# Kernel optimization log

Measured on AMD Instinct MI355X. Metric: run time of the kernel, lower is better.

The kernel has to match this reference:

```python
import jax, jax.numpy as jnp
from jax import lax
import numpy as np

N_STEPS = 6  # fixed-grid dopri5 steps over t in [0,1] (stands in for adaptive solve at rtol=atol=1e-3)
EPS = 1e-5


def group_norm(x, w, b, groups=32):
    B, C, H, W = x.shape
    xr = x.reshape(B, groups, -1)
    m = xr.mean(-1, keepdims=True)
    v = xr.var(-1, keepdims=True)
    xn = ((xr - m) * lax.rsqrt(v + EPS)).reshape(B, C, H, W)
    return xn * w[None, :, None, None] + b[None, :, None, None]


def conv2d(x, w, b, stride, pad):
    y = lax.conv_general_dilated(x, w, (stride, stride), [(pad, pad), (pad, pad)],
                                 dimension_numbers=('NCHW', 'OIHW', 'NCHW'))
    return y + b[None, :, None, None]


def make_odefunc(oa_w, oa_b, occ1_w, occ1_b, ob_w, ob_b, occ2_w, occ2_b, oc_w, oc_b):
    def f(t, x):
        B, _, H, W = x.shape
        tt = jnp.full((B, 1, H, W), t, x.dtype)
        h = jax.nn.relu(group_norm(x, oa_w, oa_b))
        h = conv2d(jnp.concatenate([tt, h], axis=1), occ1_w, occ1_b, 1, 1)
        h = jax.nn.relu(group_norm(h, ob_w, ob_b))
        h = conv2d(jnp.concatenate([tt, h], axis=1), occ2_w, occ2_b, 1, 1)
        return group_norm(h, oc_w, oc_b)
    return f


def dopri5_fixed(f, y0, t0=0.0, t1=1.0, n=N_STEPS):
    h = (t1 - t0) / n
    def step(y, i):
        t = t0 + i * h
        k1 = f(t, y)
        k2 = f(t + h * (1/5),  y + h * (1/5) * k1)
        k3 = f(t + h * (3/10), y + h * ((3/40) * k1 + (9/40) * k2))
        k4 = f(t + h * (4/5),  y + h * ((44/45) * k1 + (-56/15) * k2 + (32/9) * k3))
        k5 = f(t + h * (8/9),  y + h * ((19372/6561) * k1 + (-25360/2187) * k2 + (64448/6561) * k3 + (-212/729) * k4))
        k6 = f(t + h,          y + h * ((9017/3168) * k1 + (-355/33) * k2 + (46732/5247) * k3 + (49/176) * k4 + (-5103/18656) * k5))
        y1 = y + h * ((35/384) * k1 + (500/1113) * k3 + (125/192) * k4 + (-2187/6784) * k5 + (11/84) * k6)
        return y1, None
    y, _ = lax.scan(step, y0, jnp.arange(n, dtype=jnp.float32))
    return y


def setup_inputs() -> dict:
    key = jax.random.key(0)
    ks = jax.random.split(key, 8)
    d = {}
    d['x'] = jax.random.normal(ks[0], (256, 3, 32, 32), jnp.float32)
    d['c1_w'] = jax.random.normal(ks[1], (64, 3, 3, 3), jnp.float32) * 0.1
    d['c1_b'] = jnp.zeros((64,), jnp.float32)
    d['g1_w'] = jnp.ones((64,), jnp.float32); d['g1_b'] = jnp.zeros((64,), jnp.float32)
    d['c2_w'] = jax.random.normal(ks[2], (64, 64, 4, 4), jnp.float32) * 0.05
    d['c2_b'] = jnp.zeros((64,), jnp.float32)
    d['g2_w'] = jnp.ones((64,), jnp.float32); d['g2_b'] = jnp.zeros((64,), jnp.float32)
    d['c3_w'] = jax.random.normal(ks[3], (64, 64, 4, 4), jnp.float32) * 0.05
    d['c3_b'] = jnp.zeros((64,), jnp.float32)
    d['oa_w'] = jnp.ones((64,), jnp.float32); d['oa_b'] = jnp.zeros((64,), jnp.float32)
    d['occ1_w'] = jax.random.normal(ks[4], (64, 65, 3, 3), jnp.float32) * 0.05
    d['occ1_b'] = jnp.zeros((64,), jnp.float32)
    d['ob_w'] = jnp.ones((64,), jnp.float32); d['ob_b'] = jnp.zeros((64,), jnp.float32)
    d['occ2_w'] = jax.random.normal(ks[5], (64, 65, 3, 3), jnp.float32) * 0.05
    d['occ2_b'] = jnp.zeros((64,), jnp.float32)
    d['oc_w'] = jnp.ones((64,), jnp.float32); d['oc_b'] = jnp.zeros((64,), jnp.float32)
    d['g3_w'] = jnp.ones((64,), jnp.float32); d['g3_b'] = jnp.zeros((64,), jnp.float32)
    d['lin_w'] = jax.random.normal(ks[6], (10, 64), jnp.float32) * 0.1
    d['lin_b'] = jnp.zeros((10,), jnp.float32)
    return d


def reference(x, c1_w, c1_b, g1_w, g1_b, c2_w, c2_b, g2_w, g2_b, c3_w, c3_b,
              oa_w, oa_b, occ1_w, occ1_b, ob_w, ob_b, occ2_w, occ2_b, oc_w, oc_b,
              g3_w, g3_b, lin_w, lin_b):
    h = jax.nn.relu(group_norm(conv2d(x, c1_w, c1_b, 1, 0), g1_w, g1_b))   # [B,64,30,30]
    h = jax.nn.relu(group_norm(conv2d(h, c2_w, c2_b, 2, 1), g2_w, g2_b))   # [B,64,15,15]
    h = conv2d(h, c3_w, c3_b, 2, 1)                                        # [B,64,7,7]
    f = make_odefunc(oa_w, oa_b, occ1_w, occ1_b, ob_w, ob_b, occ2_w, occ2_b, oc_w, oc_b)
    h = dopri5_fixed(f, h)                                                 # ODE solve t:0->1
    h = jax.nn.relu(group_norm(h, g3_w, g3_b))
    h = h.mean(axis=(2, 3))                                                # adaptive avg pool (1,1) + flatten
    return h @ lin_w.T + lin_b                                             # [B,10]
```

## Files before the change

kernel.cpp:

```cpp
#include <hip/hip_runtime.h>
#include <hip/hip_bf16.h>

#define B 256
#define NELEM 3136
#define TOTAL (B*NELEM)

typedef __attribute__((ext_vector_type(8))) short bf16x8;
typedef __attribute__((ext_vector_type(4))) float f32x4;

#define MFMA16(a,b,c) __builtin_amdgcn_mfma_f32_16x16x32_bf16((a),(b),(c),0,0,0)

__device__ __forceinline__ unsigned short f2bf(float f) {
    unsigned u = __float_as_uint(f);
    unsigned r = (u + 0x7fffu + ((u >> 16) & 1u)) >> 16;
    return (unsigned short)r;
}
__device__ __forceinline__ unsigned int f2bf2(float lo, float hi) {
    return (unsigned int)f2bf(lo) | ((unsigned int)f2bf(hi) << 16);
}

__device__ const int d_sigma[64] = {
    6,12,13,19,0,20,1,7,2,8,3,9,4,10,5,11,
    18,24,25,31,26,32,27,33,14,34,15,21,16,22,17,23,
    30,36,37,43,38,44,39,45,40,46,41,47,28,48,29,35,
    42,42,42,42,42,42,42,42,42,42,42,42,42,42,42,42
};

__global__ __launch_bounds__(256) void prep_afrag_kernel(
    const float* __restrict__ w1, const float* __restrict__ w2,
    short* __restrict__ af1, short* __restrict__ af2)
{
    const int e = blockIdx.x * 256 + threadIdx.x;
    const float* W = blockIdx.y ? w2 : w1;
    short* dst = blockIdx.y ? af2 : af1;
    const int j = e & 7;
    const int lane = (e >> 3) & 63;
    const int kt = (e >> 9) % 18;
    const int mt = (e >> 9) / 18;
    const int m = mt*16 + (lane & 15);
    const int k = kt*32 + ((lane >> 4) & 3)*8 + j;
    const int tap = k >> 6;
    const int ic  = k & 63;
    dst[e] = (short)f2bf(W[m*585 + (ic + 1)*9 + tap]);
}

__global__ __launch_bounds__(256) void prep_stab_kernel(
    const float* __restrict__ w1, const float* __restrict__ w2,
    float* __restrict__ stab1, float* __restrict__ stab2)
{
    const int id = blockIdx.x * 256 + threadIdx.x;
    if (id >= 3136) return;
    const float* W = blockIdx.y ? w2 : w1;
    float* dst = blockIdx.y ? stab2 : stab1;
    const int oc = id / 49, p = id % 49;
    const int py = p / 7, px = p % 7;
    float s = 0.f;
    #pragma unroll
    for (int ky = 0; ky < 3; ++ky) {
        int iy = py - 1 + ky;
        if (iy < 0 || iy > 6) continue;
        #pragma unroll
        for (int kx = 0; kx < 3; ++kx) {
            int ix = px - 1 + kx;
            if (ix < 0 || ix > 6) continue;
            s += W[oc*585 + ky*3 + kx];
        }
    }
    dst[id] = s;
}

__global__ __launch_bounds__(256) void prep_c1frag_kernel(
    const float* __restrict__ w1, short* __restrict__ afc1)
{
    const int e = blockIdx.x * 256 + threadIdx.x;
    const int j = e & 7, lane = (e >> 3) & 63, mtq = e >> 9;
    const int m = mtq*16 + (lane & 15);
    const int k = ((lane >> 4) & 3)*8 + j;
    float v = (k < 27) ? w1[m*27 + k] : 0.f;
    afc1[e] = (short)f2bf(v);
}

__global__ __launch_bounds__(256) void prep_c23frag_kernel(
    const float* __restrict__ w2, const float* __restrict__ w3,
    short* __restrict__ afc2, short* __restrict__ afc3)
{
    const int e = blockIdx.x * 256 + threadIdx.x;
    const float* W = blockIdx.y ? w3 : w2;
    short* dst = blockIdx.y ? afc3 : afc2;
    const int j = e & 7, lane = (e >> 3) & 63, kt = (e >> 9) & 31, mtq = e >> 14;
    const int m = mtq*16 + (lane & 15);
    const int k = kt*32 + ((lane >> 4) & 3)*8 + j;
    const int tap = k >> 6, ic = k & 63;
    dst[e] = (short)f2bf(W[m*1024 + ic*16 + tap]);
}

__global__ __launch_bounds__(512, 1) void conv1_fused(
    const float* __restrict__ x, const short* __restrict__ afc1,
    const float* __restrict__ bias,
    const float* __restrict__ g1w, const float* __restrict__ g1b,
    short* __restrict__ h1pad)
{
    __shared__ float xs[3072];
    __shared__ float gnred[128], gnq[128];
    __shared__ float s_mean[32], s_rstd[32];

    const int t = threadIdx.x, b = blockIdx.x;
    const int w = t >> 6, l = t & 63, lhi = (l >> 4) & 3, llo = l & 15;
    const int mt = w & 3, sub = w >> 2;
    const int oc0 = mt*16 + lhi*4;

    for (int i = t; i < 3072; i += 512) xs[i] = x[b*3072 + i];

    bf16x8 afr = *(const bf16x8*)(afc1 + ((size_t)(mt*64 + l))*8);

    int boff[8]; bool bval[8];
    #pragma unroll
    for (int j = 0; j < 8; ++j) {
        int k = lhi*8 + j;
        bval[j] = (k < 27);
        int kk = bval[j] ? k : 0;
        int c = kk / 9, tap = kk % 9;
        boff[j] = c*1024 + (tap/3)*32 + (tap%3);
    }
    f32x4 bia = *(const f32x4*)&bias[oc0];
    __syncthreads();

    f32x4 acc[29];
    float s[4] = {0,0,0,0}, q[4] = {0,0,0,0};
    #pragma unroll
    for (int i = 0; i < 29; ++i) {
        const int nt = sub*29 + i;
        f32x4 a = {0.f,0.f,0.f,0.f};
        if (nt < 57) {
            const int p = nt*16 + llo;
            const int pc = p < 900 ? p : 899;
            const int base = (pc/30)*32 + (pc%30);
            union { bf16x8 v; unsigned u[4]; } bb;
            #pragma unroll
            for (int jj = 0; jj < 4; ++jj) {
                float e0 = bval[2*jj]   ? xs[boff[2*jj]   + base] : 0.f;
                float e1 = bval[2*jj+1] ? xs[boff[2*jj+1] + base] : 0.f;
                bb.u[jj] = f2bf2(e0, e1);
            }
            a = MFMA16(afr, bb.v, a);
            #pragma unroll
            for (int r = 0; r < 4; ++r) {
                a[r] += bia[r];
                if (p < 900) { s[r] += a[r]; q[r] += a[r]*a[r]; }
            }
        }
        acc[i] = a;
    }

    #pragma unroll
    for (int off = 1; off < 16; off <<= 1) {
        #pragma unroll
        for (int r = 0; r < 4; ++r) {
            s[r] += __shfl_xor(s[r], off);
            q[r] += __shfl_xor(q[r], off);
        }
    }
    if (llo == 0) {
        #pragma unroll
        for (int r = 0; r < 4; ++r) {
            gnred[w*16 + lhi*4 + r] = s[r];
            gnq[w*16 + lhi*4 + r]   = q[r];
        }
    }
    __syncthreads();
    if (t < 32) {
        const int oc = t*2;
// ... 71 lines not shown
    f32x4 bia = *(const f32x4*)&bias[oc0];
    __syncthreads();

    f32x4 acc[8];
    #pragma unroll
    for (int i = 0; i < 8; ++i) acc[i] = (f32x4){0.f,0.f,0.f,0.f};

    #pragma unroll
    for (int i = 0; i < 8; ++i) {
        const int nt = half*8 + i;
        if (nt > 14) continue;
        const int n = nt*16 + llo;
        const int p = n < 225 ? n : 224;
        const int oy = p/15, ox = p%15;
        #pragma unroll
        for (int kt = 0; kt < 32; ++kt) {
            const int tap = kt >> 1;
            const int ky = tap >> 2, kx = tap & 3;
            const int pidx = (oy*2 + ky)*32 + (ox*2 + kx);
            const int c8 = (kt & 1)*4 + lhi;
            bf16x8 bb = *(const bf16x8*)(sin + c8*16400 + pidx*16);
            acc[i] = MFMA16(aw[kt], bb, acc[i]);
        }
    }

    float s[4] = {0,0,0,0}, q[4] = {0,0,0,0};
    #pragma unroll
    for (int i = 0; i < 8; ++i) {
        const int nt = half*8 + i;
        if (nt > 14) continue;
        const int n = nt*16 + llo;
        #pragma unroll
        for (int r = 0; r < 4; ++r) {
            float v = acc[i][r] + bia[r];
            acc[i][r] = v;
            if (n < 225) { s[r] += v; q[r] += v*v; }
        }
    }
    #pragma unroll
    for (int off = 1; off < 16; off <<= 1) {
        #pragma unroll
        for (int r = 0; r < 4; ++r) {
            s[r] += __shfl_xor(s[r], off);
            q[r] += __shfl_xor(q[r], off);
        }
    }
    if (llo == 0) {
        #pragma unroll
        for (int r = 0; r < 4; ++r) {
            gnred[w*16 + lhi*4 + r] = s[r];
            gnq[w*16 + lhi*4 + r]   = q[r];
        }
    }
    __syncthreads();
    if (t < 32) {
        const int oc = t*2;
        const int mtg = oc >> 4, lh = (oc >> 2) & 3, r0 = oc & 3;
        const int i0 = (mtg*2)*16 + lh*4 + r0;
        float ss = gnred[i0] + gnred[i0+1] + gnred[i0+16] + gnred[i0+17];
        float qq = gnq[i0]   + gnq[i0+1]   + gnq[i0+16]   + gnq[i0+17];
        float m = ss * (1.f/450.f);
        float var = qq * (1.f/450.f) - m*m;
        s_mean[t] = m; s_rstd[t] = rsqrtf(var + 1e-5f);
    }
    __syncthreads();

    const int g0 = oc0 >> 1;
    const float m0 = s_mean[g0],   rs0 = s_rstd[g0];
    const float m1 = s_mean[g0+1], rs1 = s_rstd[g0+1];
    const float w0 = g2w[oc0], w1v = g2w[oc0+1], w2v = g2w[oc0+2], w3v = g2w[oc0+3];
    const float b0 = g2b[oc0], b1v_ = g2b[oc0+1], b2v_ = g2b[oc0+2], b3v_ = g2b[oc0+3];
    char* hb2 = (char*)h2pad + (size_t)b*36992;

    #pragma unroll
    for (int i = 0; i < 8; ++i) {
        const int nt = half*8 + i;
        if (nt > 14) continue;
        const int n = nt*16 + llo;
        if (n >= 225) continue;
        const int pidx = (n/15 + 1)*17 + (n%15 + 1);
        float v0 = fmaxf((acc[i][0]-m0)*rs0*w0  + b0,   0.f);
        float v1 = fmaxf((acc[i][1]-m0)*rs0*w1v + b1v_, 0.f);
        float v2 = fmaxf((acc[i][2]-m1)*rs1*w2v + b2v_, 0.f);
        float v3 = fmaxf((acc[i][3]-m1)*rs1*w3v + b3v_, 0.f);
        uint2 pk; pk.x = f2bf2(v0, v1); pk.y = f2bf2(v2, v3);
        *(uint2*)(hb2 + (oc0>>3)*4624 + pidx*16 + ((oc0&7)<<1)) = pk;
    }
    if (t < 512) {
        const int bp = t >> 3, c8 = t & 7;
        int pidx;
        if (bp < 17) pidx = bp;
        else if (bp < 34) pidx = 16*17 + (bp - 17);
        else if (bp < 49) pidx = (bp - 34 + 1)*17;
        else pidx = (bp - 49 + 1)*17 + 16;
        uint4 z; z.x = z.y = z.z = z.w = 0u;
        *(uint4*)(hb2 + c8*4624 + pidx*16) = z;
    }
}

__global__ __launch_bounds__(512, 1) void conv3_mfma(
    const short* __restrict__ h2pad, const short* __restrict__ afc3,
    const float* __restrict__ bias, float* __restrict__ y)
{
    __shared__ __align__(16) char sin[36992];
    const int t = threadIdx.x, b = blockIdx.x;
    const int w = t >> 6, l = t & 63, lhi = (l >> 4) & 3, llo = l & 15;
    const int mt = w >> 1, half = w & 1;
    const int oc0 = mt*16 + lhi*4;

    {
        const uint4* src = (const uint4*)((const char*)h2pad + (size_t)b*36992);
        uint4* dst = (uint4*)sin;
        for (int i = t; i < 2312; i += 512) dst[i] = src[i];
    }
    bf16x8 aw[32];
    #pragma unroll
    for (int kt = 0; kt < 32; ++kt)
        aw[kt] = *(const bf16x8*)(afc3 + ((size_t)((mt*32 + kt)*64 + l))*8);
    f32x4 bia = *(const f32x4*)&bias[oc0];
    __syncthreads();

    f32x4 acc[2];
    acc[0] = (f32x4){0.f,0.f,0.f,0.f};
    acc[1] = (f32x4){0.f,0.f,0.f,0.f};
    #pragma unroll
    for (int i = 0; i < 2; ++i) {
        const int nt = half*2 + i;
        const int n = nt*16 + llo;
        const int p = n < 49 ? n : 48;
        const int oy = p/7, ox = p%7;
        #pragma unroll
        for (int kt = 0; kt < 32; ++kt) {
            const int tap = kt >> 1;
            const int ky = tap >> 2, kx = tap & 3;
            const int pidx = (oy*2 + ky)*17 + (ox*2 + kx);
            const int c8 = (kt & 1)*4 + lhi;
            bf16x8 bb = *(const bf16x8*)(sin + c8*4624 + pidx*16);
            acc[i] = MFMA16(aw[kt], bb, acc[i]);
        }
    }
    #pragma unroll
    for (int i = 0; i < 2; ++i) {
        const int n = (half*2 + i)*16 + llo;
        if (n < 49) {
            #pragma unroll
            for (int r = 0; r < 4; ++r)
                y[(size_t)b*NELEM + (oc0 + r)*49 + n] = acc[i][r] + bia[r];
        }
    }
}

#define SGRP 104
#define KSTR 3328
#define ODE_LDS 115456
__global__ __launch_bounds__(512, 1) void ode_head(
    const float* __restrict__ yin,
    const short* __restrict__ af1, const short* __restrict__ af2,
    const float* __restrict__ stab1, const float* __restrict__ stab2,
    const float* __restrict__ b1v, const float* __restrict__ b2v,
    const float* __restrict__ oaw, const float* __restrict__ oab,
    const float* __restrict__ obw, const float* __restrict__ obb,
    const float* __restrict__ ocw, const float* __restrict__ ocb,
    const float* __restrict__ g3w, const float* __restrict__ g3b,
    const float* __restrict__ linw, const float* __restrict__ linb,
    float* __restrict__ out)
{
    extern __shared__ char smem[];
    float* y_l    = (float*)smem;
    float* kbuf   = (float*)(smem + 13312);
    char*  act0   = smem + 93184;
    char*  act1   = smem + 103552;
    float* gnred  = (float*)(smem + 113920);
    float* soaw   = (float*)(smem + 114432);
    float* soab   = (float*)(smem + 114688);
    float* s_mean = (float*)(smem + 114944);
    float* s_rstd = (float*)(smem + 115072);
    float* s_cm   = (float*)(smem + 115200);

    const int t = threadIdx.x, b = blockIdx.x;
    const int w = t >> 6, l = t & 63, lhi = (l >> 4) & 3, llo = l & 15;
    const int mt = w >> 1;
    const int ntA = (w & 1)*2, ntB = ntA + 1;
    const int nA = ntA*16 + llo, nB = ntB*16 + llo;
    const bool vA = nA < 49, vB = nB < 49;
    const int pxA = d_sigma[nA], pxB = d_sigma[nB];
    const int paA = (pxA/7 + 1)*9 + (pxA%7 + 1);
    const int paB = (pxB/7 + 1)*9 + (pxB%7 + 1);
    const int oc0 = mt*16 + lhi*4;
    const int g16 = t >> 4, sub = t & 15;

    for (int u = t; u < 3136; u += 512) {
        const int g = u / 98, e = u - g*98;
        y_l[g*SGRP + e] = yin[(size_t)b*NELEM + u];
    }
    for (int i = t; i < 5184; i += 512) ((unsigned*)act0)[i] = 0u;
    if (t < 64) { soaw[t] = oaw[t]; soab[t] = oab[t]; }

    float stabA1[4], stabB1[4], stabA2[4], stabB2[4];
    #pragma unroll
    for (int r = 0; r < 4; ++r) {
        stabA1[r] = stab1[(oc0 + r)*49 + pxA];
        stabB1[r] = stab1[(oc0 + r)*49 + pxB];
        stabA2[r] = stab2[(oc0 + r)*49 + pxA];
        stabB2[r] = stab2[(oc0 + r)*49 + pxB];
    }
    const f32x4 bia1 = *(const f32x4*)&b1v[oc0];
    const f32x4 bia2 = *(const f32x4*)&b2v[oc0];
    const f32x4 gwB = *(const f32x4*)&obw[oc0];
    const f32x4 gbB = *(const f32x4*)&obb[oc0];
    const f32x4 gwC = *(const f32x4*)&ocw[oc0];
    const f32x4 gbC = *(const f32x4*)&ocb[oc0];
    __syncthreads();

    const float hf  = (float)(1.0/6.0);
    const float C10 = (float)((1.0/6.0)*(1.0/5.0));
    const float C20 = (float)((1.0/6.0)*(3.0/40.0)),  C21 = (float)((1.0/6.0)*(9.0/40.0));
    const float C30 = (float)((1.0/6.0)*(44.0/45.0)), C31 = (float)((1.0/6.0)*(-56.0/15.0)), C32 = (float)((1.0/6.0)*(32.0/9.0));
    const float C40 = (float)((1.0/6.0)*(19372.0/6561.0)), C41 = (float)((1.0/6.0)*(-25360.0/2187.0)),
                C42 = (float)((1.0/6.0)*(64448.0/6561.0)), C43 = (float)((1.0/6.0)*(-212.0/729.0));
    const float C50 = (float)((1.0/6.0)*(9017.0/3168.0)), C51 = (float)((1.0/6.0)*(-355.0/33.0)),
                C52 = (float)((1.0/6.0)*(46732.0/5247.0)), C53 = (float)((1.0/6.0)*(49.0/176.0)),
                C54 = (float)((1.0/6.0)*(-5103.0/18656.0));
    const float B0 = (float)((1.0/6.0)*(35.0/384.0)), B2c = (float)((1.0/6.0)*(500.0/1113.0)),
                B3c = (float)((1.0/6.0)*(125.0/192.0)), B4c = (float)((1.0/6.0)*(-2187.0/6784.0)),
                B5c = (float)((1.0/6.0)*(11.0/84.0));

    for (int step = 0; step < 6; ++step) {
        const float t0 = (float)step * hf;
        for (int stage = 0; stage < 6; ++stage) {
            float cA=0.f, cB=0.f, cC=0.f, cD=0.f, cE=0.f, tf=0.f;
            if (stage == 1)      { cA=C10; tf = 0.2f; }
            else if (stage == 2) { cA=C20; cB=C21; tf = 0.3f; }
            else if (stage == 3) { cA=C30; cB=C31; cC=C32; tf = 0.8f; }
            else if (stage == 4) { cA=C40; cB=C41; cC=C42; cD=C43; tf = (float)(8.0/9.0); }
            else if (stage == 5) { cA=C50; cB=C51; cC=C52; cD=C53; cE=C54; tf = 1.f; }
            const float tval = t0 + hf*tf;

            {
                const float* Yg = y_l + g16*SGRP;
                const float* Kg = kbuf + g16*SGRP;
                const int e0 = 4*sub;
                const int n1 = (sub < 8) ? 4 : ((sub == 8) ? 2 : 0);
                const int e1 = 64 + 4*sub;

                f32x4 va, vb = {0.f,0.f,0.f,0.f};
                {
                    f32x4 xv = *(const f32x4*)(Yg + e0);
                    if (stage > 0) xv += cA * *(const f32x4*)(Kg + 0*KSTR + e0);
                    if (stage > 1) xv += cB * *(const f32x4*)(Kg + 1*KSTR + e0);
                    if (stage > 2) xv += cC * *(const f32x4*)(Kg + 2*KSTR + e0);
                    if (stage > 3) xv += cD * *(const f32x4*)(Kg + 3*KSTR + e0);
                    if (stage > 4) xv += cE * *(const f32x4*)(Kg + 4*KSTR + e0);
                    va = xv;
                }
                if (n1 == 4) {
                    f32x4 xv = *(const f32x4*)(Yg + e1);
                    if (stage > 0) xv += cA * *(const f32x4*)(Kg + 0*KSTR + e1);
                    if (stage > 1) xv += cB * *(const f32x4*)(Kg + 1*KSTR + e1);
                    if (stage > 2) xv += cC * *(const f32x4*)(Kg + 2*KSTR + e1);
                    if (stage > 3) xv += cD * *(const f32x4*)(Kg + 3*KSTR + e1);
                    if (stage > 4) xv += cE * *(const f32x4*)(Kg + 4*KSTR + e1);
                    vb = xv;
                } else if (n1 == 2) {
                    float x0 = Yg[96], x1 = Yg[97];
                    if (stage > 0) { x0 = fmaf(cA, Kg[0*KSTR+96], x0); x1 = fmaf(cA, Kg[0*KSTR+97], x1); }
                    if (stage > 1) { x0 = fmaf(cB, Kg[1*KSTR+96], x0); x1 = fmaf(cB, Kg[1*KSTR+97], x1); }
                    if (stage > 2) { x0 = fmaf(cC, Kg[2*KSTR+96], x0); x1 = fmaf(cC, Kg[2*KSTR+97], x1); }
                    if (stage > 3) { x0 = fmaf(cD, Kg[3*KSTR+96], x0); x1 = fmaf(cD, Kg[3*KSTR+97], x1); }
                    if (stage > 4) { x0 = fmaf(cE, Kg[4*KSTR+96], x0); x1 = fmaf(cE, Kg[4*KSTR+97], x1); }
                    vb[0] = x0; vb[1] = x1;
                }

                float s = va[0]+va[1]+va[2]+va[3];
                float q = va[0]*va[0]+va[1]*va[1]+va[2]*va[2]+va[3]*va[3];
                if (n1 >= 2) { s += vb[0]+vb[1]; q += vb[0]*vb[0]+vb[1]*vb[1]; }
                if (n1 == 4) { s += vb[2]+vb[3]; q += vb[2]*vb[2]+vb[3]*vb[3]; }
                s += __shfl_xor(s, 1); q += __shfl_xor(q, 1);
                s += __shfl_xor(s, 2); q += __shfl_xor(q, 2);
                s += __shfl_xor(s, 4); q += __shfl_xor(q, 4);
                s += __shfl_xor(s, 8); q += __shfl_xor(q, 8);
                const float m = s * (1.f/98.f);
                const float rs = rsqrtf(q * (1.f/98.f) - m*m + 1e-5f);
                const float w0 = soaw[2*g16], w1s = soaw[2*g16+1];
                const float bb0 = soab[2*g16], bb1 = soab[2*g16+1];

                #pragma unroll
                for (int j2 = 0; j2 < 4; ++j2) {
                    const int e = e0 + j2;
                    const int odd = e >= 49 ? 1 : 0;
                    const int ch = 2*g16 + odd;
                    const int p = e - 49*odd;
                    float nv = fmaxf((va[j2] - m)*rs*(odd ? w1s : w0) + (odd ? bb1 : bb0), 0.f);
                    const int pa = (p/7 + 1)*9 + (p%7) + 1;
                    *(unsigned short*)(act0 + (ch>>3)*1296 + pa*16 + ((ch&7)<<1)) = f2bf(nv);
                }
                for (int j2 = 0; j2 < n1; ++j2) {
                    const int e = e1 + j2;
                    const int odd = e >= 49 ? 1 : 0;
                    const int ch = 2*g16 + odd;
                    const int p = e - 49*odd;
                    float nv = fmaxf((vb[j2] - m)*rs*(odd ? w1s : w0) + (odd ? bb1 : bb0), 0.f);
                    const int pa = (p/7 + 1)*9 + (p%7) + 1;
                    *(unsigned short*)(act0 + (ch>>3)*1296 + pa*16 + ((ch&7)<<1)) = f2bf(nv);
                }
            }
            __syncthreads();

            float v0[4], v1[4];
            {
                bf16x8 aw[18];
                #pragma unroll
                for (int kt = 0; kt < 18; ++kt)
                    aw[kt] = *(const bf16x8*)(af1 + ((size_t)(mt*18 + kt)*64 + l)*8);
                f32x4 acc0 = {0.f,0.f,0.f,0.f}, acc1 = {0.f,0.f,0.f,0.f};
                #pragma unroll
                for (int kt = 0; kt < 18; ++kt) {
                    const int tap = kt >> 1;
                    const int dB = ((tap/3 - 1)*9 + (tap%3 - 1))*16;
                    const int cb = ((kt & 1)*4 + lhi)*1296;
                    bf16x8 bb0 = *(const bf16x8*)(act0 + cb + paA*16 + dB);
                    bf16x8 bb1 = *(const bf16x8*)(act0 + cb + paB*16 + dB);
                    acc0 = MFMA16(aw[kt], bb0, acc0);
                    acc1 = MFMA16(aw[kt], bb1, acc1);
                }
                #pragma unroll
                for (int r = 0; r < 4; ++r) {
                    v0[r] = acc0[r] + bia1[r] + tval * stabA1[r];
                    v1[r] = acc1[r] + bia1[r] + tval * stabB1[r];
                }
            }
            {
                float s0=0.f,q0=0.f,s1=0.f,q1=0.f;
                if (vA) { s0 += v0[0]+v0[1]; q0 += v0[0]*v0[0]+v0[1]*v0[1];
                          s1 += v0[2]+v0[3]; q1 += v0[2]*v0[2]+v0[3]*v0[3]; }
                if (vB) { s0 += v1[0]+v1[1]; q0 += v1[0]*v1[0]+v1[1]*v1[1];
                          s1 += v1[2]+v1[3]; q1 += v1[2]*v1[2]+v1[3]*v1[3]; }
                #pragma unroll
                for (int off = 1; off < 16; off <<= 1) {
                    s0 += __shfl_xor(s0, off); q0 += __shfl_xor(q0, off);
                    s1 += __shfl_xor(s1, off); q1 += __shfl_xor(q1, off);
                }
                if (llo == 0) {
                    float* gp = gnred + w*16 + lhi*4;
                    gp[0]=s0; gp[1]=q0; gp[2]=s1; gp[3]=q1;
                }
            }
            __syncthreads();
            {
                const int gb = mt*32 + lhi*4;
                const float sg0 = gnred[gb]   + gnred[gb+16];
                const float qg0 = gnred[gb+1] + gnred[gb+17];
                const float sg1 = gnred[gb+2] + gnred[gb+18];
                const float qg1 = gnred[gb+3] + gnred[gb+19];
                const float m0 = sg0*(1.f/98.f);
                const float r0 = rsqrtf(qg0*(1.f/98.f) - m0*m0 + 1e-5f);
                const float m1 = sg1*(1.f/98.f);
                const float r1 = rsqrtf(qg1*(1.f/98.f) - m1*m1 + 1e-5f);
                v0[0] = fmaxf((v0[0]-m0)*r0*gwB[0]+gbB[0], 0.f);
                v0[1] = fmaxf((v0[1]-m0)*r0*gwB[1]+gbB[1], 0.f);
                v0[2] = fmaxf((v0[2]-m1)*r1*gwB[2]+gbB[2], 0.f);
                v0[3] = fmaxf((v0[3]-m1)*r1*gwB[3]+gbB[3], 0.f);
                v1[0] = fmaxf((v1[0]-m0)*r0*gwB[0]+gbB[0], 0.f);
                v1[1] = fmaxf((v1[1]-m0)*r0*gwB[1]+gbB[1], 0.f);
                v1[2] = fmaxf((v1[2]-m1)*r1*gwB[2]+gbB[2], 0.f);
                v1[3] = fmaxf((v1[3]-m1)*r1*gwB[3]+gbB[3], 0.f);
                if (vA) {
                    uint2 pk; pk.x = f2bf2(v0[0], v0[1]); pk.y = f2bf2(v0[2], v0[3]);
                    *(uint2*)(act1 + (oc0>>3)*1296 + paA*16 + ((oc0&7)<<1)) = pk;
                }
                if (vB) {
                    uint2 pk; pk.x = f2bf2(v1[0], v1[1]); pk.y = f2bf2(v1[2], v1[3]);
                    *(uint2*)(act1 + (oc0>>3)*1296 + paB*16 + ((oc0&7)<<1)) = pk;
                }
            }
            __syncthreads();

            {
                bf16x8 aw[18];
                #pragma unroll
                for (int kt = 0; kt < 18; ++kt)
                    aw[kt] = *(const bf16x8*)(af2 + ((size_t)(mt*18 + kt)*64 + l)*8);
                f32x4 acc0 = {0.f,0.f,0.f,0.f}, acc1 = {0.f,0.f,0.f,0.f};
                #pragma unroll
                for (int kt = 0; kt < 18; ++kt) {
                    const int tap = kt >> 1;
                    const int dB = ((tap/3 - 1)*9 + (tap%3 - 1))*16;
                    const int cb = ((kt & 1)*4 + lhi)*1296;
                    bf16x8 bb0 = *(const bf16x8*)(act1 + cb + paA*16 + dB);
                    bf16x8 bb1 = *(const bf16x8*)(act1 + cb + paB*16 + dB);
                    acc0 = MFMA16(aw[kt], bb0, acc0);
                    acc1 = MFMA16(aw[kt], bb1, acc1);
                }
                #pragma unroll
                for (int r = 0; r < 4; ++r) {
                    v0[r] = acc0[r] + bia2[r] + tval * stabA2[r];
                    v1[r] = acc1[r] + bia2[r] + tval * stabB2[r];
                }
            }
            {
                float s0=0.f,q0=0.f,s1=0.f,q1=0.f;
                if (vA) { s0 += v0[0]+v0[1]; q0 += v0[0]*v0[0]+v0[1]*v0[1];
                          s1 += v0[2]+v0[3]; q1 += v0[2]*v0[2]+v0[3]*v0[3]; }
                if (vB) { s0 += v1[0]+v1[1]; q0 += v1[0]*v1[0]+v1[1]*v1[1];
                          s1 += v1[2]+v1[3]; q1 += v1[2]*v1[2]+v1[3]*v1[3]; }
                #pragma unroll
                for (int off = 1; off < 16; off <<= 1) {
                    s0 += __shfl_xor(s0, off); q0 += __shfl_xor(q0, off);
                    s1 += __shfl_xor(s1, off); q1 += __shfl_xor(q1, off);
                }
                if (llo == 0) {
                    float* gp = gnred + w*16 + lhi*4;
                    gp[0]=s0; gp[1]=q0; gp[2]=s1; gp[3]=q1;
                }
            }
            __syncthreads();
            {
                const int gb = mt*32 + lhi*4;
                const float sg0 = gnred[gb]   + gnred[gb+16];
                const float qg0 = gnred[gb+1] + gnred[gb+17];
                const float sg1 = gnred[gb+2] + gnred[gb+18];
                const float qg1 = gnred[gb+3] + gnred[gb+19];
                const float m0 = sg0*(1.f/98.f);
                const float r0 = rsqrtf(qg0*(1.f/98.f) - m0*m0 + 1e-5f);
                const float m1 = sg1*(1.f/98.f);
                const float r1 = rsqrtf(qg1*(1.f/98.f) - m1*m1 + 1e-5f);
                float* kd = kbuf + stage*KSTR;
                const int gA = oc0 >> 1;
                if (vA) {
                    kd[gA*SGRP + pxA]            = (v0[0]-m0)*r0*gwC[0]+gbC[0];
                    kd[gA*SGRP + 49 + pxA]       = (v0[1]-m0)*r0*gwC[1]+gbC[1];
                    kd[(gA+1)*SGRP + pxA]        = (v0[2]-m1)*r1*gwC[2]+gbC[2];
                    kd[(gA+1)*SGRP + 49 + pxA]   = (v0[3]-m1)*r1*gwC[3]+gbC[3];
                }
                if (vB) {
                    kd[gA*SGRP + pxB]            = (v1[0]-m0)*r0*gwC[0]+gbC[0];
                    kd[gA*SGRP + 49 + pxB]       = (v1[1]-m0)*r0*gwC[1]+gbC[1];
                    kd[(gA+1)*SGRP + pxB]        = (v1[2]-m1)*r1*gwC[2]+gbC[2];
                    kd[(gA+1)*SGRP + 49 + pxB]   = (v1[3]-m1)*r1*gwC[3]+gbC[3];
                }
            }
            __syncthreads();

            if (stage == 5) {
                float* Yg = y_l + g16*SGRP;
                const float* Kg = kbuf + g16*SGRP;
                const int e0 = 4*sub;
                {
                    f32x4 v = *(const f32x4*)(Yg + e0);
                    v += B0  * *(const f32x4*)(Kg + 0*KSTR + e0);
                    v += B2c * *(const f32x4*)(Kg + 2*KSTR + e0);
                    v += B3c * *(const f32x4*)(Kg + 3*KSTR + e0);
                    v += B4c * *(const f32x4*)(Kg + 4*KSTR + e0);
                    v += B5c * *(const f32x4*)(Kg + 5*KSTR + e0);
                    *(f32x4*)(Yg + e0) = v;
                }
                if (sub < 8) {
                    const int e1 = 64 + 4*sub;
                    f32x4 v = *(const f32x4*)(Yg + e1);
                    v += B0  * *(const f32x4*)(Kg + 0*KSTR + e1);
                    v += B2c * *(const f32x4*)(Kg + 2*KSTR + e1);
                    v += B3c * *(const f32x4*)(Kg + 3*KSTR + e1);
                    v += B4c * *(const f32x4*)(Kg + 4*KSTR + e1);
                    v += B5c * *(const f32x4*)(Kg + 5*KSTR + e1);
                    *(f32x4*)(Yg + e1) = v;
                } else if (sub == 8) {
                    #pragma unroll
                    for (int j2 = 0; j2 < 2; ++j2) {
                        const int e = 96 + j2;
                        float v = Yg[e];
                        v = fmaf(B0,  Kg[0*KSTR+e], v);
                        v = fmaf(B2c, Kg[2*KSTR+e], v);
                        v = fmaf(B3c, Kg[3*KSTR+e], v);
                        v = fmaf(B4c, Kg[4*KSTR+e], v);
                        v = fmaf(B5c, Kg[5*KSTR+e], v);
                        Yg[e] = v;
                    }
                }
                __syncthreads();
            }
        }
    }

    {
        float s = 0.f, q = 0.f;
        const float* Yg = y_l + g16*SGRP;
        for (int e = sub; e < 98; e += 16) {
            float v = Yg[e];
            s += v; q += v*v;
        }
        s += __shfl_xor(s,1); q += __shfl_xor(q,1);
        s += __shfl_xor(s,2); q += __shfl_xor(q,2);
        s += __shfl_xor(s,4); q += __shfl_xor(q,4);
        s += __shfl_xor(s,8); q += __shfl_xor(q,8);
        if (sub == 0) {
            float m = s * (1.f/98.f);
            float var = q * (1.f/98.f) - m*m;
            s_mean[g16] = m; s_rstd[g16] = rsqrtf(var + 1e-5f);
        }
    }
    __syncthreads();
    if (t < 64) {
        const int ch = t, g = ch >> 1;
        const float m = s_mean[g], r = s_rstd[g];
        const float ww = g3w[ch], bb = g3b[ch];
        const float* Yc = y_l + g*SGRP + (ch & 1)*49;
        float sum = 0.f;
        for (int p = 0; p < 49; ++p) {
            float v = (Yc[p] - m)*r*ww + bb;
            sum += fmaxf(v, 0.f);
        }
        s_cm[ch] = sum * (1.f/49.f);
    }
    __syncthreads();
    if (t < 10) {
        float a = linb[t];
        for (int c = 0; c < 64; ++c) a = fmaf(s_cm[c], linw[t*64 + c], a);
        out[b*10 + t] = a;
    }
}

extern "C" void kernel_launch(void* const* d_in, const int* in_sizes, int n_in,
                              void* d_out, int out_size, void* d_ws, size_t ws_size,
                              hipStream_t stream)
{
    const float* x      = (const float*)d_in[0];
    const float* c1_w   = (const float*)d_in[1];
    const float* c1_b   = (const float*)d_in[2];
    const float* g1_w   = (const float*)d_in[3];
    const float* g1_b   = (const float*)d_in[4];
    const float* c2_w   = (const float*)d_in[5];
    const float* c2_b   = (const float*)d_in[6];
    const float* g2_w   = (const float*)d_in[7];
    const float* g2_b   = (const float*)d_in[8];
    const float* c3_w   = (const float*)d_in[9];
    const float* c3_b   = (const float*)d_in[10];
    const float* oa_w   = (const float*)d_in[11];
    const float* oa_b   = (const float*)d_in[12];
    const float* occ1_w = (const float*)d_in[13];
    const float* occ1_b = (const float*)d_in[14];
    const float* ob_w   = (const float*)d_in[15];
    const float* ob_b   = (const float*)d_in[16];
    const float* occ2_w = (const float*)d_in[17];
    const float* occ2_b = (const float*)d_in[18];
    const float* oc_w   = (const float*)d_in[19];
    const float* oc_b   = (const float*)d_in[20];
    const float* g3_w   = (const float*)d_in[21];
    const float* g3_b   = (const float*)d_in[22];
    const float* lin_w  = (const float*)d_in[23];
    const float* lin_b  = (const float*)d_in[24];
    float* out = (float*)d_out;

    float* ws = (float*)d_ws;
    size_t off = 0;
    float* y     = ws + off; off += 802816;
    float* stab1 = ws + off; off += 3136;
    float* stab2 = ws + off; off += 3136;
    short* af1   = (short*)(ws + off); off += 18432;
    short* af2   = (short*)(ws + off); off += 18432;
    short* afc1  = (short*)(ws + off); off += 1024;
    short* afc2  = (short*)(ws + off); off += 32768;
    short* afc3  = (short*)(ws + off); off += 32768;
    short* h1pad = (short*)(ws + off); off += 8396800;
    short* h2pad = (short*)(ws + off); off += 2367488;

    prep_afrag_kernel<<<dim3(144, 2), 256, 0, stream>>>(occ1_w, occ2_w, af1, af2);
    prep_stab_kernel<<<dim3(13, 2), 256, 0, stream>>>(occ1_w, occ2_w, stab1, stab2);
    prep_c1frag_kernel<<<8, 256, 0, stream>>>(c1_w, afc1);
    prep_c23frag_kernel<<<dim3(256, 2), 256, 0, stream>>>(c2_w, c3_w, afc2, afc3);

    conv1_fused<<<B, 512, 0, stream>>>(x, afc1, c1_b, g1_w, g1_b, h1pad);
    conv2_fused<<<B, 512, CONV2_LDS, stream>>>(h1pad, afc2, c2_b, g2_w, g2_b, h2pad);
    conv3_mfma<<<B, 512, 0, stream>>>(h2pad, afc3, c3_b, y);

    ode_head<<<B, 512, ODE_LDS, stream>>>(y, af1, af2, stab1, stab2,
        occ1_b, occ2_b, oa_w, oa_b, ob_w, ob_b, oc_w, oc_b,
        g3_w, g3_b, lin_w, lin_b, out);
}
```

Before: 251.7 us.

## Remap ODE conv waves to two output-channel tiles sharing one activation fragment

```diff
diff --git a/kernel.cpp b/kernel.cpp
--- a/kernel.cpp
+++ b/kernel.cpp
@@ -5,8 +5,8 @@
 #define NELEM 3136
 #define TOTAL (B*NELEM)
 
-typedef __attribute__((ext_vector_type(8))) short bf16x8;
-typedef __attribute__((ext_vector_type(4))) float f32x4;
+typedef __attribute__((ext_vector_type(8)))  short bf16x8;
+typedef __attribute__((ext_vector_type(4)))  float f32x4;
 
 #define MFMA16(a,b,c) __builtin_amdgcn_mfma_f32_16x16x32_bf16((a),(b),(c),0,0,0)
 
@@ -17,6 +17,11 @@
 }
 __device__ __forceinline__ unsigned int f2bf2(float lo, float hi) {
     return (unsigned int)f2bf(lo) | ((unsigned int)f2bf(hi) << 16);
+}
+__device__ __forceinline__ unsigned int cvtpk(float lo, float hi) {
+    unsigned int r;
+    asm("v_cvt_pk_bf16_f32 %0, %1, %2" : "=v"(r) : "v"(lo), "v"(hi));
+    return r;
 }
 
 __device__ const int d_sigma[64] = {
@@ -394,8 +399,17 @@
 
 #define SGRP 104
 #define KSTR 3328
-#define ODE_LDS 115456
-__global__ __launch_bounds__(512, 1) void ode_head(
+#define ACT_C8 1296
+#define ODE_LDS 117248
+#define P_B1 0
+#define P_B2 64
+#define P_GWB 128
+#define P_GBB 192
+#define P_GWC 256
+#define P_GBC 320
+#define P_OAW 384
+#define P_OAB 448
+__global__ __launch_bounds__(512, 2) void ode_head(
     const float* __restrict__ yin,
     const short* __restrict__ af1, const short* __restrict__ af2,
     const float* __restrict__ stab1, const float* __restrict__ stab2,
@@ -408,50 +422,46 @@
     float* __restrict__ out)
 {
     extern __shared__ char smem[];
-    float* y_l    = (float*)smem;
-    float* kbuf   = (float*)(smem + 13312);
-    char*  act0   = smem + 93184;
-    char*  act1   = smem + 103552;
-    float* gnred  = (float*)(smem + 113920);
-    float* soaw   = (float*)(smem + 114432);
-    float* soab   = (float*)(smem + 114688);
-    float* s_mean = (float*)(smem + 114944);
-    float* s_rstd = (float*)(smem + 115072);
-    float* s_cm   = (float*)(smem + 115200);
+    float* y_l   = (float*)smem;
+    float* kbuf  = (float*)(smem + 13312);
+    char*  act0  = smem + 93184;
+    char*  act1  = smem + 103552;
+    float* prm   = (float*)(smem + 113920);
+    float* gnred = (float*)(smem + 115968);
+    float* s_cm  = (float*)(smem + 116992);
 
     const int t = threadIdx.x, b = blockIdx.x;
     const int w = t >> 6, l = t & 63, lhi = (l >> 4) & 3, llo = l & 15;
-    const int mt = w >> 1;
-    const int ntA = (w & 1)*2, ntB = ntA + 1;
-    const int nA = ntA*16 + llo, nB = ntB*16 + llo;
-    const bool vA = nA < 49, vB = nB < 49;
-    const int pxA = d_sigma[nA], pxB = d_sigma[nB];
-    const int paA = (pxA/7 + 1)*9 + (pxA%7 + 1);
-    const int paB = (pxB/7 + 1)*9 + (pxB%7 + 1);
-    const int oc0 = mt*16 + lhi*4;
     const int g16 = t >> 4, sub = t & 15;
+
+    const int ms = w >> 2, np = w & 3;
+    const int n  = np*16 + llo;
+    const bool vpx = n < 49;
+    const int px = d_sigma[n];
+    const int pa = (px/7 + 1)*9 + (px%7 + 1);
+    const int mt0 = 2*ms, mt1 = 2*ms + 1;
 
     for (int u = t; u < 3136; u += 512) {
         const int g = u / 98, e = u - g*98;
         y_l[g*SGRP + e] = yin[(size_t)b*NELEM + u];
     }
     for (int i = t; i < 5184; i += 512) ((unsigned*)act0)[i] = 0u;
-    if (t < 64) { soaw[t] = oaw[t]; soab[t] = oab[t]; }
-
-    float stabA1[4], stabB1[4], stabA2[4], stabB2[4];
-    #pragma unroll
-    for (int r = 0; r < 4; ++r) {
-        stabA1[r] = stab1[(oc0 + r)*49 + pxA];
-        stabB1[r] = stab1[(oc0 + r)*49 + pxB];
-        stabA2[r] = stab2[(oc0 + r)*49 + pxA];
-        stabB2[r] = stab2[(oc0 + r)*49 + pxB];
-    }
-    const f32x4 bia1 = *(const f32x4*)&b1v[oc0];
-    const f32x4 bia2 = *(const f32x4*)&b2v[oc0];
-    const f32x4 gwB = *(const f32x4*)&obw[oc0];
-    const f32x4 gbB = *(const f32x4*)&obb[oc0];
-    const f32x4 gwC = *(const f32x4*)&ocw[oc0];
-    const f32x4 gbC = *(const f32x4*)&ocb[oc0];
+    if (t < 64) {
+        prm[P_B1  + t] = b1v[t]; prm[P_B2  + t] = b2v[t];
+        prm[P_GWB + t] = obw[t]; prm[P_GBB + t] = obb[t];
+        prm[P_GWC + t] = ocw[t]; prm[P_GBC + t] = ocb[t];
+        prm[P_OAW + t] = oaw[t]; prm[P_OAB + t] = oab[t];
+    }
+    float st1[2][4], st2[2][4];
+    #pragma unroll
+    for (int s = 0; s < 2; ++s) {
+        const int ocs = (2*ms + s)*16 + lhi*4;
+        #pragma unroll
+        for (int r = 0; r < 4; ++r) {
+            st1[s][r] = stab1[(ocs + r)*49 + px];
+            st2[s][r] = stab2[(ocs + r)*49 + px];
+        }
+    }
     __syncthreads();
 
     const float hf  = (float)(1.0/6.0);
@@ -477,6 +487,13 @@
             else if (stage == 4) { cA=C40; cB=C41; cC=C42; cD=C43; tf = (float)(8.0/9.0); }
             else if (stage == 5) { cA=C50; cB=C51; cC=C52; cD=C53; cE=C54; tf = 1.f; }
             const float tval = t0 + hf*tf;
+
+            bf16x8 aw[2][18];
+            #pragma unroll
+            for (int kt = 0; kt < 18; ++kt) {
+                aw[0][kt] = *(const bf16x8*)(af1 + ((size_t)(mt0*18 + kt)*64 + l)*8);
+                aw[1][kt] = *(const bf16x8*)(af1 + ((size_t)(mt1*18 + kt)*64 + l)*8);
+            }
 
             {
                 const float* Yg = y_l + g16*SGRP;
@@ -523,8 +540,8 @@
                 s += __shfl_xor(s, 8); q += __shfl_xor(q, 8);
                 const float m = s * (1.f/98.f);
                 const float rs = rsqrtf(q * (1.f/98.f) - m*m + 1e-5f);
-                const float w0 = soaw[2*g16], w1s = soaw[2*g16+1];
-                const float bb0 = soab[2*g16], bb1 = soab[2*g16+1];
+                const float w0 = prm[P_OAW + 2*g16], w1c = prm[P_OAW + 2*g16 + 1];
+                const float c0 = prm[P_OAB + 2*g16], c1c = prm[P_OAB + 2*g16 + 1];
 
                 #pragma unroll
                 for (int j2 = 0; j2 < 4; ++j2) {
@@ -532,153 +549,157 @@
                     const int odd = e >= 49 ? 1 : 0;
                     const int ch = 2*g16 + odd;
                     const int p = e - 49*odd;
-                    float nv = fmaxf((va[j2] - m)*rs*(odd ? w1s : w0) + (odd ? bb1 : bb0), 0.f);
-                    const int pa = (p/7 + 1)*9 + (p%7) + 1;
-                    *(unsigned short*)(act0 + (ch>>3)*1296 + pa*16 + ((ch&7)<<1)) = f2bf(nv);
+                    float nv = fmaxf((va[j2] - m)*rs*(odd ? w1c : w0) + (odd ? c1c : c0), 0.f);
+                    const int pw = (p/7 + 1)*9 + (p%7) + 1;
+                    *(unsigned short*)(act0 + (ch>>3)*ACT_C8 + pw*16 + ((ch&7)<<1)) = f2bf(nv);
                 }
                 for (int j2 = 0; j2 < n1; ++j2) {
                     const int e = e1 + j2;
                     const int odd = e >= 49 ? 1 : 0;
                     const int ch = 2*g16 + odd;
                     const int p = e - 49*odd;
-                    float nv = fmaxf((vb[j2] - m)*rs*(odd ? w1s : w0) + (odd ? bb1 : bb0), 0.f);
-                    const int pa = (p/7 + 1)*9 + (p%7) + 1;
-                    *(unsigned short*)(act0 + (ch>>3)*1296 + pa*16 + ((ch&7)<<1)) = f2bf(nv);
+                    float nv = fmaxf((vb[j2] - m)*rs*(odd ? w1c : w0) + (odd ? c1c : c0), 0.f);
+                    const int pw = (p/7 + 1)*9 + (p%7) + 1;
+                    *(unsigned short*)(act0 + (ch>>3)*ACT_C8 + pw*16 + ((ch&7)<<1)) = f2bf(nv);
                 }
             }
             __syncthreads();
 
-            float v0[4], v1[4];
+            float v0[2][4];
             {
-                bf16x8 aw[18];
-                #pragma unroll
-                for (int kt = 0; kt < 18; ++kt)
-                    aw[kt] = *(const bf16x8*)(af1 + ((size_t)(mt*18 + kt)*64 + l)*8);
-                f32x4 acc0 = {0.f,0.f,0.f,0.f}, acc1 = {0.f,0.f,0.f,0.f};
+                f32x4 a0 = {0.f,0.f,0.f,0.f}, a1 = {0.f,0.f,0.f,0.f};
                 #pragma unroll
                 for (int kt = 0; kt < 18; ++kt) {
                     const int tap = kt >> 1;
                     const int dB = ((tap/3 - 1)*9 + (tap%3 - 1))*16;
-                    const int cb = ((kt & 1)*4 + lhi)*1296;
-                    bf16x8 bb0 = *(const bf16x8*)(act0 + cb + paA*16 + dB);
-                    bf16x8 bb1 = *(const bf16x8*)(act0 + cb + paB*16 + dB);
-                    acc0 = MFMA16(aw[kt], bb0, acc0);
-                    acc1 = MFMA16(aw[kt], bb1, acc1);
+                    const int cb = ((kt & 1)*4 + lhi)*ACT_C8;
+                    bf16x8 bb = *(const bf16x8*)(act0 + cb + pa*16 + dB);
+                    a0 = MFMA16(aw[0][kt], bb, a0);
+                    a1 = MFMA16(aw[1][kt], bb, a1);
                 }
                 #pragma unroll
-                for (int r = 0; r < 4; ++r) {
-                    v0[r] = acc0[r] + bia1[r] + tval * stabA1[r];
-                    v1[r] = acc1[r] + bia1[r] + tval * stabB1[r];
-                }
-            }
-            {
+                for (int kt = 0; kt < 18; ++kt) {
+                    aw[0][kt] = *(const bf16x8*)(af2 + ((size_t)(mt0*18 + kt)*64 + l)*8);
+                    aw[1][kt] = *(const bf16x8*)(af2 + ((size_t)(mt1*18 + kt)*64 + l)*8);
+                }
+                #pragma unroll
+                for (int s = 0; s < 2; ++s) {
+                    const int ocs = (2*ms + s)*16 + lhi*4;
+                    f32x4 bia = *(const f32x4*)&prm[P_B1 + ocs];
+                    #pragma unroll
+                    for (int r = 0; r < 4; ++r)
+                        v0[s][r] = (s ? a1[r] : a0[r]) + bia[r] + tval * st1[s][r];
+                }
+            }
+            #pragma unroll
+            for (int s = 0; s < 2; ++s) {
                 float s0=0.f,q0=0.f,s1=0.f,q1=0.f;
-                if (vA) { s0 += v0[0]+v0[1]; q0 += v0[0]*v0[0]+v0[1]*v0[1];
-                          s1 += v0[2]+v0[3]; q1 += v0[2]*v0[2]+v0[3]*v0[3]; }
-                if (vB) { s0 += v1[0]+v1[1]; q0 += v1[0]*v1[0]+v1[1]*v1[1];
-                          s1 += v1[2]+v1[3]; q1 += v1[2]*v1[2]+v1[3]*v1[3]; }
-                #pragma unroll
-                for (int off = 1; off < 16; off <<= 1) {
-                    s0 += __shfl_xor(s0, off); q0 += __shfl_xor(q0, off);
-                    s1 += __shfl_xor(s1, off); q1 += __shfl_xor(q1, off);
-                }
+                if (vpx) {
+                    s0 = v0[s][0]+v0[s][1]; q0 = v0[s][0]*v0[s][0]+v0[s][1]*v0[s][1];
+                    s1 = v0[s][2]+v0[s][3]; q1 = v0[s][2]*v0[s][2]+v0[s][3]*v0[s][3];
+                }
+                s0 += __shfl_xor(s0,1); q0 += __shfl_xor(q0,1); s1 += __shfl_xor(s1,1); q1 += __shfl_xor(q1,1);
+                s0 += __shfl_xor(s0,2); q0 += __shfl_xor(q0,2); s1 += __shfl_xor(s1,2); q1 += __shfl_xor(q1,2);
+                s0 += __shfl_xor(s0,4); q0 += __shfl_xor(q0,4); s1 += __shfl_xor(s1,4); q1 += __shfl_xor(q1,4);
+                s0 += __shfl_xor(s0,8); q0 += __shfl_xor(q0,8); s1 += __shfl_xor(s1,8); q1 += __shfl_xor(q1,8);
                 if (llo == 0) {
-                    float* gp = gnred + w*16 + lhi*4;
-                    gp[0]=s0; gp[1]=q0; gp[2]=s1; gp[3]=q1;
+                    const int p0 = (2*ms + s)*8 + lhi*2;
+                    gnred[p0*8 + np*2]         = s0;
+                    gnred[p0*8 + np*2 + 1]     = q0;
+                    gnred[(p0+1)*8 + np*2]     = s1;
+                    gnred[(p0+1)*8 + np*2 + 1] = q1;
                 }
             }
             __syncthreads();
-            {
-                const int gb = mt*32 + lhi*4;
-                const float sg0 = gnred[gb]   + gnred[gb+16];
-                const float qg0 = gnred[gb+1] + gnred[gb+17];
-                const float sg1 = gnred[gb+2] + gnred[gb+18];
-                const float qg1 = gnred[gb+3] + gnred[gb+19];
+
+            #pragma unroll
+            for (int s = 0; s < 2; ++s) {
+                const int ocs = (2*ms + s)*16 + lhi*4;
+                const int p0 = ocs >> 1;
+                const float sg0 = gnred[p0*8]+gnred[p0*8+2]+gnred[p0*8+4]+gnred[p0*8+6];
+                const float qg0 = gnred[p0*8+1]+gnred[p0*8+3]+gnred[p0*8+5]+gnred[p0*8+7];
+                const float sg1 = gnred[(p0+1)*8]+gnred[(p0+1)*8+2]+gnred[(p0+1)*8+4]+gnred[(p0+1)*8+6];
+                const float qg1 = gnred[(p0+1)*8+1]+gnred[(p0+1)*8+3]+gnred[(p0+1)*8+5]+gnred[(p0+1)*8+7];
                 const float m0 = sg0*(1.f/98.f);
                 const float r0 = rsqrtf(qg0*(1.f/98.f) - m0*m0 + 1e-5f);
                 const float m1 = sg1*(1.f/98.f);
                 const float r1 = rsqrtf(qg1*(1.f/98.f) - m1*m1 + 1e-5f);
-                v0[0] = fmaxf((v0[0]-m0)*r0*gwB[0]+gbB[0], 0.f);
-                v0[1] = fmaxf((v0[1]-m0)*r0*gwB[1]+gbB[1], 0.f);
-                v0[2] = fmaxf((v0[2]-m1)*r1*gwB[2]+gbB[2], 0.f);
-                v0[3] = fmaxf((v0[3]-m1)*r1*gwB[3]+gbB[3], 0.f);
-                v1[0] = fmaxf((v1[0]-m0)*r0*gwB[0]+gbB[0], 0.f);
-                v1[1] = fmaxf((v1[1]-m0)*r0*gwB[1]+gbB[1], 0.f);
-                v1[2] = fmaxf((v1[2]-m1)*r1*gwB[2]+gbB[2], 0.f);
-                v1[3] = fmaxf((v1[3]-m1)*r1*gwB[3]+gbB[3], 0.f);
-                if (vA) {
-                    uint2 pk; pk.x = f2bf2(v0[0], v0[1]); pk.y = f2bf2(v0[2], v0[3]);
-                    *(uint2*)(act1 + (oc0>>3)*1296 + paA*16 + ((oc0&7)<<1)) = pk;
-                }
-                if (vB) {
-                    uint2 pk; pk.x = f2bf2(v1[0], v1[1]); pk.y = f2bf2(v1[2], v1[3]);
-                    *(uint2*)(act1 + (oc0>>3)*1296 + paB*16 + ((oc0&7)<<1)) = pk;
+                f32x4 gw = *(const f32x4*)&prm[P_GWB + ocs];
+                f32x4 gc = *(const f32x4*)&prm[P_GBB + ocs];
+                if (vpx) {
+                    float x0 = fmaxf((v0[s][0]-m0)*r0*gw[0]+gc[0], 0.f);
+                    float x1 = fmaxf((v0[s][1]-m0)*r0*gw[1]+gc[1], 0.f);
+                    float x2 = fmaxf((v0[s][2]-m1)*r1*gw[2]+gc[2], 0.f);
+                    float x3 = fmaxf((v0[s][3]-m1)*r1*gw[3]+gc[3], 0.f);
+                    uint2 pk; pk.x = cvtpk(x0, x1); pk.y = cvtpk(x2, x3);
+                    *(uint2*)(act1 + (ocs>>3)*ACT_C8 + pa*16 + ((ocs&7)<<1)) = pk;
                 }
             }
             __syncthreads();
 
             {
-                bf16x8 aw[18];
-                #pragma unroll
-                for (int kt = 0; kt < 18; ++kt)
-                    aw[kt] = *(const bf16x8*)(af2 + ((size_t)(mt*18 + kt)*64 + l)*8);
-                f32x4 acc0 = {0.f,0.f,0.f,0.f}, acc1 = {0.f,0.f,0.f,0.f};
+                f32x4 a0 = {0.f,0.f,0.f,0.f}, a1 = {0.f,0.f,0.f,0.f};
                 #pragma unroll
                 for (int kt = 0; kt < 18; ++kt) {
                     const int tap = kt >> 1;
                     const int dB = ((tap/3 - 1)*9 + (tap%3 - 1))*16;
-                    const int cb = ((kt & 1)*4 + lhi)*1296;
-                    bf16x8 bb0 = *(const bf16x8*)(act1 + cb + paA*16 + dB);
-                    bf16x8 bb1 = *(const bf16x8*)(act1 + cb + paB*16 + dB);
-                    acc0 = MFMA16(aw[kt], bb0, acc0);
-                    acc1 = MFMA16(aw[kt], bb1, acc1);
+                    const int cb = ((kt & 1)*4 + lhi)*ACT_C8;
+                    bf16x8 bb = *(const bf16x8*)(act1 + cb + pa*16 + dB);
+                    a0 = MFMA16(aw[0][kt], bb, a0);
+                    a1 = MFMA16(aw[1][kt], bb, a1);
                 }
                 #pragma unroll
-                for (int r = 0; r < 4; ++r) {
-                    v0[r] = acc0[r] + bia2[r] + tval * stabA2[r];
-                    v1[r] = acc1[r] + bia2[r] + tval * stabB2[r];
-                }
-            }
+                for (int s = 0; s < 2; ++s) {
+                    const int ocs = (2*ms + s)*16 + lhi*4;
+                    f32x4 bia = *(const f32x4*)&prm[P_B2 + ocs];
+                    #pragma unroll
+                    for (int r = 0; r < 4; ++r)
+                        v0[s][r] = (s ? a1[r] : a0[r]) + bia[r] + tval * st2[s][r];
+                }
+            }
+            #pragma unroll
+            for (int s = 0; s < 2; ++s) {
+                float s0=0.f,q0=0.f,s1=0.f,q1=0.f;
+                if (vpx) {
+                    s0 = v0[s][0]+v0[s][1]; q0 = v0[s][0]*v0[s][0]+v0[s][1]*v0[s][1];
+                    s1 = v0[s][2]+v0[s][3]; q1 = v0[s][2]*v0[s][2]+v0[s][3]*v0[s][3];
+                }
+                s0 += __shfl_xor(s0,1); q0 += __shfl_xor(q0,1); s1 += __shfl_xor(s1,1); q1 += __shfl_xor(q1,1);
+                s0 += __shfl_xor(s0,2); q0 += __shfl_xor(q0,2); s1 += __shfl_xor(s1,2); q1 += __shfl_xor(q1,2);
+                s0 += __shfl_xor(s0,4); q0 += __shfl_xor(q0,4); s1 += __shfl_xor(s1,4); q1 += __shfl_xor(q1,4);
+                s0 += __shfl_xor(s0,8); q0 += __shfl_xor(q0,8); s1 += __shfl_xor(s1,8); q1 += __shfl_xor(q1,8);
+                if (llo == 0) {
+                    const int p0 = (2*ms + s)*8 + lhi*2;
+                    gnred[p0*8 + np*2]         = s0;
+                    gnred[p0*8 + np*2 + 1]     = q0;
+                    gnred[(p0+1)*8 + np*2]     = s1;
+                    gnred[(p0+1)*8 + np*2 + 1] = q1;
+                }
+            }
+            __syncthreads();
+
             {
-                float s0=0.f,q0=0.f,s1=0.f,q1=0.f;
-                if (vA) { s0 += v0[0]+v0[1]; q0 += v0[0]*v0[0]+v0[1]*v0[1];
-                          s1 += v0[2]+v0[3]; q1 += v0[2]*v0[2]+v0[3]*v0[3]; }
-                if (vB) { s0 += v1[0]+v1[1]; q0 += v1[0]*v1[0]+v1[1]*v1[1];
-                          s1 += v1[2]+v1[3]; q1 += v1[2]*v1[2]+v1[3]*v1[3]; }
+                float* kd = kbuf + stage*KSTR;
                 #pragma unroll
-                for (int off = 1; off < 16; off <<= 1) {
-                    s0 += __shfl_xor(s0, off); q0 += __shfl_xor(q0, off);
-                    s1 += __shfl_xor(s1, off); q1 += __shfl_xor(q1, off);
-                }
-                if (llo == 0) {
-                    float* gp = gnred + w*16 + lhi*4;
-                    gp[0]=s0; gp[1]=q0; gp[2]=s1; gp[3]=q1;
-                }
-            }
-            __syncthreads();
-            {
-                const int gb = mt*32 + lhi*4;
-                const float sg0 = gnred[gb]   + gnred[gb+16];
-                const float qg0 = gnred[gb+1] + gnred[gb+17];
-                const float sg1 = gnred[gb+2] + gnred[gb+18];
-                const float qg1 = gnred[gb+3] + gnred[gb+19];
-                const float m0 = sg0*(1.f/98.f);
-                const float r0 = rsqrtf(qg0*(1.f/98.f) - m0*m0 + 1e-5f);
-                const float m1 = sg1*(1.f/98.f);
-                const float r1 = rsqrtf(qg1*(1.f/98.f) - m1*m1 + 1e-5f);
-                float* kd = kbuf + stage*KSTR;
-                const int gA = oc0 >> 1;
-                if (vA) {
-                    kd[gA*SGRP + pxA]            = (v0[0]-m0)*r0*gwC[0]+gbC[0];
-                    kd[gA*SGRP + 49 + pxA]       = (v0[1]-m0)*r0*gwC[1]+gbC[1];
-                    kd[(gA+1)*SGRP + pxA]        = (v0[2]-m1)*r1*gwC[2]+gbC[2];
-                    kd[(gA+1)*SGRP + 49 + pxA]   = (v0[3]-m1)*r1*gwC[3]+gbC[3];
-                }
-                if (vB) {
-                    kd[gA*SGRP + pxB]            = (v1[0]-m0)*r0*gwC[0]+gbC[0];
-                    kd[gA*SGRP + 49 + pxB]       = (v1[1]-m0)*r0*gwC[1]+gbC[1];
-                    kd[(gA+1)*SGRP + pxB]        = (v1[2]-m1)*r1*gwC[2]+gbC[2];
-                    kd[(gA+1)*SGRP + 49 + pxB]   = (v1[3]-m1)*r1*gwC[3]+gbC[3];
+                for (int s = 0; s < 2; ++s) {
+                    const int ocs = (2*ms + s)*16 + lhi*4;
+                    const int p0 = ocs >> 1;
+                    const float sg0 = gnred[p0*8]+gnred[p0*8+2]+gnred[p0*8+4]+gnred[p0*8+6];
+                    const float qg0 = gnred[p0*8+1]+gnred[p0*8+3]+gnred[p0*8+5]+gnred[p0*8+7];
+                    const float sg1 = gnred[(p0+1)*8]+gnred[(p0+1)*8+2]+gnred[(p0+1)*8+4]+gnred[(p0+1)*8+6];
+                    const float qg1 = gnred[(p0+1)*8+1]+gnred[(p0+1)*8+3]+gnred[(p0+1)*8+5]+gnred[(p0+1)*8+7];
+                    const float m0 = sg0*(1.f/98.f);
+                    const float r0 = rsqrtf(qg0*(1.f/98.f) - m0*m0 + 1e-5f);
+                    const float m1 = sg1*(1.f/98.f);
+                    const float r1 = rsqrtf(qg1*(1.f/98.f) - m1*m1 + 1e-5f);
+                    f32x4 gw = *(const f32x4*)&prm[P_GWC + ocs];
+                    f32x4 gc = *(const f32x4*)&prm[P_GBC + ocs];
+                    if (vpx) {
+                        kd[p0*SGRP + px]          = (v0[s][0]-m0)*r0*gw[0]+gc[0];
+                        kd[p0*SGRP + 49 + px]     = (v0[s][1]-m0)*r0*gw[1]+gc[1];
+                        kd[(p0+1)*SGRP + px]      = (v0[s][2]-m1)*r1*gw[2]+gc[2];
+                        kd[(p0+1)*SGRP + 49 + px] = (v0[s][3]-m1)*r1*gw[3]+gc[3];
+                    }
                 }
             }
             __syncthreads();
@@ -723,6 +744,7 @@
         }
     }
 
+    float* hstat = kbuf;
     {
         float s = 0.f, q = 0.f;
         const float* Yg = y_l + g16*SGRP;
@@ -737,13 +759,13 @@
         if (sub == 0) {
             float m = s * (1.f/98.f);
             float var = q * (1.f/98.f) - m*m;
-            s_mean[g16] = m; s_rstd[g16] = rsqrtf(var + 1e-5f);
+            hstat[g16] = m; hstat[32 + g16] = rsqrtf(var + 1e-5f);
         }
     }
     __syncthreads();
     if (t < 64) {
         const int ch = t, g = ch >> 1;
-        const float m = s_mean[g], r = s_rstd[g];
+        const float m = hstat[g], r = hstat[32 + g];
         const float ww = g3w[ch], bb = g3b[ch];
         const float* Yc = y_l + g*SGRP + (ch & 1)*49;
         float sum = 0.f;
```

Measured after the change: 752.0 us. 199% more time.
